# Optimization experiments

Hardware: AMD Instinct MI355X
Metric: run time of the kernel (lower is better)

## Reference

```python
import jax, jax.numpy as jnp
import numpy as np

NEG_SLOPE = 0.01  # torch LeakyReLU default

def setup_inputs() -> dict:
    key = jax.random.key(0)
    ks = jax.random.split(key, 16)
    B, T = 256, 168
    LAG, LAT, WS, H = 168, 128, 64, 1024
    def lin(kw, kb, out_f, in_f):
        bound = 1.0 / np.sqrt(in_f)
        W = jax.random.uniform(kw, (out_f, in_f), jnp.float32, -bound, bound)
        b = jax.random.uniform(kb, (out_f,), jnp.float32, -bound, bound)
        return W, b
    W1, b1 = lin(ks[0], ks[1], 64, LAG)
    W2, b2 = lin(ks[2], ks[3], LAT, 64)
    W3, b3 = lin(ks[4], ks[5], H, LAT)
    bound = 1.0 / np.sqrt(H)
    Wih = jax.random.uniform(ks[6], (3 * H, WS), jnp.float32, -bound, bound)
    Whh = jax.random.uniform(ks[7], (3 * H, H), jnp.float32, -bound, bound)
    bih = jax.random.uniform(ks[8], (3 * H,), jnp.float32, -bound, bound)
    bhh = jax.random.uniform(ks[9], (3 * H,), jnp.float32, -bound, bound)
    Wo, bo = lin(ks[10], ks[11], 1, H)
    lag = jax.random.normal(ks[12], (B, LAG), jnp.float32)
    curr = jax.random.normal(ks[13], (T, B, WS), jnp.float32)
    return dict(lag=lag, curr=curr, W1=W1, b1=b1, W2=W2, b2=b2, W3=W3, b3=b3,
                Wih=Wih, Whh=Whh, bih=bih, bhh=bhh, Wo=Wo, bo=bo)

def _leaky(x):
    return jnp.where(x >= 0, x, NEG_SLOPE * x)

def reference(lag, curr, W1, b1, W2, b2, W3, b3, Wih, Whh, bih, bhh, Wo, bo):
    # Encoder MLP: lag -> 64 -> latent -> hidden (leaky relu after first two)
    h = _leaky(lag @ W1.T + b1)
    h = _leaky(h @ W2.T + b2)
    h0 = h @ W3.T + b3  # [B, H]
    H = h0.shape[-1]

    def step(h_t, x_t):
        gi = x_t @ Wih.T + bih          # [B, 3H]
        gh = h_t @ Whh.T + bhh          # [B, 3H]
        ir, iz, inn = jnp.split(gi, 3, axis=-1)
        hr, hz, hn = jnp.split(gh, 3, axis=-1)
        r = jax.nn.sigmoid(ir + hr)
        z = jax.nn.sigmoid(iz + hz)
        n = jnp.tanh(inn + r * hn)
        h_new = (1.0 - z) * n + z * h_t
        return h_new, h_new

    _, hs = jax.lax.scan(step, h0, curr)          # hs: [T, B, H]
    preds = jnp.squeeze(hs @ Wo.T + bo, -1)       # [T, B]
    return preds.T                                 # [B, T]
```

## Files before the change

### kernel.cpp

```cpp
#include <hip/hip_runtime.h>
#include <hip/hip_bf16.h>
#include <cstdint>
#include <cstddef>

typedef _Float16 half8 __attribute__((ext_vector_type(8)));
typedef _Float16 half4 __attribute__((ext_vector_type(4)));
typedef float floatx4 __attribute__((ext_vector_type(4)));
typedef unsigned long long u64;

#define B_ 256
#define T_ 168
#define H_ 1024
#define WS_ 64
#define LAG_ 168
#define LAT_ 128

__device__ __forceinline__ float fast_sigmoid(float x) {
    return __builtin_amdgcn_rcpf(1.f + __expf(-x));
}
__device__ __forceinline__ float fast_tanh(float x) {
    return 1.f - 2.f * __builtin_amdgcn_rcpf(__expf(2.f * x) + 1.f);
}

__global__ void cvt_f32_f16_v4(const float4* __restrict__ src, half4* __restrict__ dst, int n4) {
    int i = blockIdx.x * blockDim.x + threadIdx.x;
    if (i < n4) {
        float4 v = src[i];
        half4 o;
        o[0] = (_Float16)v.x; o[1] = (_Float16)v.y;
        o[2] = (_Float16)v.z; o[3] = (_Float16)v.w;
        dst[i] = o;
    }
}

__global__ void enc12(const float* __restrict__ in, const float* __restrict__ W,
                      const float* __restrict__ bias, float* __restrict__ outb, int infeat) {
    int r = blockIdx.x, j = threadIdx.x;
    const float* row = in + (size_t)r * infeat;
    const float* w   = W  + (size_t)j * infeat;
    float s = bias[j];
    for (int k = 0; k < infeat; ++k) s += row[k] * w[k];
    outb[(size_t)r * blockDim.x + j] = (s >= 0.f) ? s : 0.01f * s;
}

__global__ void enc3(const float* __restrict__ h2, const float* __restrict__ W3,
                     const float* __restrict__ b3, float* __restrict__ hprev32,
                     _Float16* __restrict__ h0f16) {
    __shared__ float s[LAT_];
    int r = blockIdx.x;
    if (threadIdx.x < LAT_) s[threadIdx.x] = h2[(size_t)r * LAT_ + threadIdx.x];
    __syncthreads();
    for (int j = threadIdx.x; j < H_; j += 256) {
        const float* w = W3 + (size_t)j * LAT_;
        float acc = b3[j];
        #pragma unroll 8
        for (int k = 0; k < LAT_; ++k) acc += s[k] * w[k];
        hprev32[(size_t)r * H_ + j] = acc;
        h0f16[(size_t)r * H_ + j]   = (_Float16)acc;
    }
}

__global__ __launch_bounds__(256, 1) void gru_persistent(
    _Float16* __restrict__ hbuf,
    const float* __restrict__ hprev32, const _Float16* __restrict__ whh16,
    const _Float16* __restrict__ wih16, const _Float16* __restrict__ x16,
    const float* __restrict__ bih, const float* __restrict__ bhh,
    const float* __restrict__ Wo, float* __restrict__ partials,
    unsigned* __restrict__ bar)
{
    __shared__ __align__(16) _Float16 Ash[16 * 1032];
    __shared__ __align__(16) _Float16 Wsh[192 * 72];
    __shared__ __align__(16) _Float16 Hsh[4 * 256];

    const int tid  = threadIdx.x;
    const int w    = tid >> 6;
    const int lane = tid & 63;
    const int m16  = lane & 15;
    const int quad = lane >> 4;
    const int pi   = blockIdx.x & 15;
    const int qi   = blockIdx.x >> 4;
    const int pi16 = pi << 4;
    const int u    = (qi << 6) + (w << 4) + m16;

    for (int idx = tid; idx < 1536; idx += 256) {
        int rowl = idx >> 3, ch = idx & 7;
        int g = rowl >> 6, ru = rowl & 63;
        *(uint4*)(&Wsh[rowl * 72 + (ch << 3)]) =
            *(const uint4*)(wih16 + (size_t)(((g << 10) + (qi << 6) + ru) << 6) + (ch << 3));
    }

    half8 br[32], bz[32];
    {
        const _Float16* p0 = whh16 + ((size_t)u << 10) + (quad << 3);
        const _Float16* p1 = whh16 + ((size_t)(H_ + u) << 10) + (quad << 3);
        #pragma unroll
        for (int c = 0; c < 32; ++c) br[c] = *(const half8*)(p0 + (c << 5));
        #pragma unroll
        for (int c = 0; c < 32; ++c) bz[c] = *(const half8*)(p1 + (c << 5));
    }
    const _Float16* bnp = whh16 + ((size_t)(2 * H_ + u) << 10) + (quad << 3);

    const float b_r  = bih[u]          + bhh[u];
    const float b_z  = bih[H_ + u]     + bhh[H_ + u];
    const float b_in = bih[2 * H_ + u];
    const float b_hn = bhh[2 * H_ + u];
    const float wo_u = Wo[u];

    float hreg[4];
    #pragma unroll
    for (int i = 0; i < 4; ++i)
        hreg[i] = hprev32[((size_t)(pi16 + (quad << 2) + i) << 10) + u];

    __syncthreads();

    unsigned* flag_self       = bar + ((((pi << 4) | qi) << 2 | w) << 4);
    const unsigned* flag_peer = bar + ((((pi << 4) | (lane >> 2)) << 2 | (lane & 3)) << 4);
    const int srow = tid >> 4;
    const int sch  = tid & 15;
    const int prow = lane >> 2;
    const int pc4  = lane & 3;

    for (int t = 0; t < T_; ++t) {
        const _Float16* hsrc = hbuf + (size_t)(t & 3) * (B_ * H_);
        _Float16*       hdst = hbuf + (size_t)((t + 1) & 3) * (B_ * H_);

        half8 ax0 = *(const half8*)(x16 + (((size_t)t << 8) + pi16 + m16) * WS_ + (quad << 3));
        half8 ax1 = *(const half8*)(x16 + (((size_t)t << 8) + pi16 + m16) * WS_ + 32 + (quad << 3));
        half8 bnA[8], bnB[8];
        #pragma unroll
        for (int j = 0; j < 8; ++j) bnA[j] = *(const half8*)(bnp + (j << 5));

        const unsigned need = (unsigned)t;
        u64 rdy = 0;

        while ((rdy & 0xFFFFull) != 0xFFFFull) {
            unsigned f = __hip_atomic_load(flag_peer, __ATOMIC_RELAXED, __HIP_MEMORY_SCOPE_AGENT);
            rdy |= __ballot(f >= need);
            if ((rdy & 0xFFFFull) != 0xFFFFull) __builtin_amdgcn_s_sleep(1);
        }
        u64 va0, va1, va2, va3;
        {
            const _Float16* s = hsrc + ((size_t)(pi16 + srow) << 10) + (sch << 4);
            va0 = __hip_atomic_load((const u64*)(s + 0),  __ATOMIC_RELAXED, __HIP_MEMORY_SCOPE_AGENT);
            va1 = __hip_atomic_load((const u64*)(s + 4),  __ATOMIC_RELAXED, __HIP_MEMORY_SCOPE_AGENT);
            va2 = __hip_atomic_load((const u64*)(s + 8),  __ATOMIC_RELAXED, __HIP_MEMORY_SCOPE_AGENT);
            va3 = __hip_atomic_load((const u64*)(s + 12), __ATOMIC_RELAXED, __HIP_MEMORY_SCOPE_AGENT);
        }

        floatx4 acc_r  = {b_r,  b_r,  b_r,  b_r };
        floatx4 acc_z  = {b_z,  b_z,  b_z,  b_z };
        floatx4 acc_in = {b_in, b_in, b_in, b_in};
        floatx4 acc_hn = {b_hn, b_hn, b_hn, b_hn};

        {
            half8 p0 = *(const half8*)(&Wsh[((w << 4) + m16) * 72        + (quad << 3)]);
            half8 p1 = *(const half8*)(&Wsh[(64 + (w << 4) + m16) * 72   + (quad << 3)]);
            half8 p2 = *(const half8*)(&Wsh[(128 + (w << 4) + m16) * 72  + (quad << 3)]);
            acc_r  = __builtin_amdgcn_mfma_f32_16x16x32_f16(ax0, p0, acc_r,  0, 0, 0);
            acc_z  = __builtin_amdgcn_mfma_f32_16x16x32_f16(ax0, p1, acc_z,  0, 0, 0);
            acc_in = __builtin_amdgcn_mfma_f32_16x16x32_f16(ax0, p2, acc_in, 0, 0, 0);
            half8 q0 = *(const half8*)(&Wsh[((w << 4) + m16) * 72        + 32 + (quad << 3)]);
            half8 q1 = *(const half8*)(&Wsh[(64 + (w << 4) + m16) * 72   + 32 + (quad << 3)]);
            half8 q2 = *(const half8*)(&Wsh[(128 + (w << 4) + m16) * 72  + 32 + (quad << 3)]);
            acc_r  = __builtin_amdgcn_mfma_f32_16x16x32_f16(ax1, q0, acc_r,  0, 0, 0);
            acc_z  = __builtin_amdgcn_mfma_f32_16x16x32_f16(ax1, q1, acc_z,  0, 0, 0);
            acc_in = __builtin_amdgcn_mfma_f32_16x16x32_f16(ax1, q2, acc_in, 0, 0, 0);
        }

        #pragma unroll
        for (int g = 0; g < 4; ++g) {
            {
                _Float16* d = &Ash[srow * 1032 + (g << 8) + (sch << 4)];
                *(u64*)(d + 0)  = va0;
                *(u64*)(d + 4)  = va1;
                *(u64*)(d + 8)  = va2;
                *(u64*)(d + 12) = va3;
            }
            __syncthreads();
            if (g < 3) {
                const u64 mask = 0xFFFFull << ((g + 1) << 4);
                while ((rdy & mask) != mask) {
                    unsigned f = __hip_atomic_load(flag_peer, __ATOMIC_RELAXED, __HIP_MEMORY_SCOPE_AGENT);
                    rdy |= __ballot(f >= need);
                    if ((rdy & mask) != mask) __builtin_amdgcn_s_sleep(1);
                }
                const _Float16* s = hsrc + ((size_t)(pi16 + srow) << 10) + ((g + 1) << 8) + (sch << 4);
                va0 = __hip_atomic_load((const u64*)(s + 0),  __ATOMIC_RELAXED, __HIP_MEMORY_SCOPE_AGENT);
                va1 = __hip_atomic_load((const u64*)(s + 4),  __ATOMIC_RELAXED, __HIP_MEMORY_SCOPE_AGENT);
                va2 = __hip_atomic_load((const u64*)(s + 8),  __ATOMIC_RELAXED, __HIP_MEMORY_SCOPE_AGENT);
                va3 = __hip_atomic_load((const u64*)(s + 12), __ATOMIC_RELAXED, __HIP_MEMORY_SCOPE_AGENT);
                #pragma unroll
                for (int j = 0; j < 8; ++j)
                    bnB[j] = *(const half8*)(bnp + ((((g + 1) << 3) + j) << 5));
            }
            #pragma unroll
            for (int j = 0; j < 8; ++j) {
                const int c = (g << 3) + j;
                half8 a = *(const half8*)(&Ash[m16 * 1032 + (c << 5) + (quad << 3)]);
                acc_r  = __builtin_amdgcn_mfma_f32_16x16x32_f16(a, br[c], acc_r,  0, 0, 0);
                acc_z  = __builtin_amdgcn_mfma_f32_16x16x32_f16(a, bz[c], acc_z,  0, 0, 0);
                acc_hn = __builtin_amdgcn_mfma_f32_16x16x32_f16(a, bnA[j], acc_hn, 0, 0, 0);
            }
            if (g < 3) {
                #pragma unroll
                for (int j = 0; j < 8; ++j) bnA[j] = bnB[j];
            }
        }

        float pv[4];
        #pragma unroll
        for (int i = 0; i < 4; ++i) {
            float rg = fast_sigmoid(acc_r[i]);
            float zg = fast_sigmoid(acc_z[i]);
            float ng = fast_tanh(acc_in[i] + rg * acc_hn[i]);
            float hn2 = (1.f - zg) * ng + zg * hreg[i];
            hreg[i] = hn2;
            pv[i] = hn2 * wo_u;
            Hsh[(w << 8) + ((quad << 2) + i) * 16 + m16] = (_Float16)hn2;
        }
        __threadfence_block();
        {
            u64 hv = *(const u64*)(&Hsh[(w << 8) + prow * 16 + (pc4 << 2)]);
            __hip_atomic_store(
                (u64*)(hdst + ((size_t)(pi16 + prow) << 10) + (qi << 6) + (w << 4) + (pc4 << 2)),
                hv, __ATOMIC_RELAXED, __HIP_MEMORY_SCOPE_AGENT);
        }
        asm volatile("s_waitcnt vmcnt(0)" ::: "memory");
        if (lane == 0)
            __hip_atomic_store(flag_self, (unsigned)(t + 1),
                               __ATOMIC_RELAXED, __HIP_MEMORY_SCOPE_AGENT);
        #pragma unroll
        for (int m = 1; m < 16; m <<= 1) {
            #pragma unroll
            for (int i = 0; i < 4; ++i) pv[i] += __shfl_xor(pv[i], m);
        }
        if (m16 == 0) {
            #pragma unroll
            for (int i = 0; i < 4; ++i)
                partials[((size_t)t * B_ + pi16 + (quad << 2) + i) * 64 + (qi << 2) + w] = pv[i];
        }
    }
}

__global__ void out_reduce(const float* __restrict__ partials, const float* __restrict__ bo,
                           float* __restrict__ out) {
    int t = blockIdx.x, r = threadIdx.x;
    const float* p = partials + ((size_t)t * B_ + r) * 64;
    float s = 0.f;
    #pragma unroll
    for (int i = 0; i < 64; ++i) s += p[i];
    out[(size_t)r * T_ + t] = s + bo[0];
}

extern "C" void kernel_launch(void* const* d_in, const int* in_sizes, int n_in,
                              void* d_out, int out_size, void* d_ws, size_t ws_size,
                              hipStream_t stream) {
    const float* lag  = (const float*)d_in[0];
    const float* curr = (const float*)d_in[1];
    const float* W1   = (const float*)d_in[2];
    const float* b1   = (const float*)d_in[3];
    const float* W2   = (const float*)d_in[4];
    const float* b2   = (const float*)d_in[5];
    const float* W3   = (const float*)d_in[6];
    const float* b3   = (const float*)d_in[7];
    const float* Wih  = (const float*)d_in[8];
    const float* Whh  = (const float*)d_in[9];
    const float* bih  = (const float*)d_in[10];
    const float* bhh  = (const float*)d_in[11];
    const float* Wo   = (const float*)d_in[12];
    const float* bo   = (const float*)d_in[13];
    float* out = (float*)d_out;

    char* ws = (char*)d_ws;
    size_t off = 0;
    auto alloc = [&](size_t bytes) -> void* {
        void* p = ws + off;
        off += (bytes + 255) & ~(size_t)255;
        return p;
    };
    _Float16* whh16 = (_Float16*)alloc((size_t)3 * H_ * H_ * 2);
    _Float16* wih16 = (_Float16*)alloc((size_t)3 * H_ * WS_ * 2);
    _Float16* x16   = (_Float16*)alloc((size_t)T_ * B_ * WS_ * 2);
    _Float16* hbuf  = (_Float16*)alloc((size_t)4 * B_ * H_ * 2);
    float* hprev32  = (float*)alloc((size_t)B_ * H_ * 4);
    float* h1       = (float*)alloc((size_t)B_ * 64 * 4);
    float* h2       = (float*)alloc((size_t)B_ * LAT_ * 4);
    float* partials = (float*)alloc((size_t)T_ * B_ * 64 * 4);
    unsigned* bar   = (unsigned*)alloc(81920);

    hipMemsetAsync(bar, 0, 81920, stream);

    int n4;
    n4 = 3 * H_ * H_ / 4;
    cvt_f32_f16_v4<<<(n4 + 255) / 256, 256, 0, stream>>>((const float4*)Whh, (half4*)whh16, n4);
    n4 = 3 * H_ * WS_ / 4;
    cvt_f32_f16_v4<<<(n4 + 255) / 256, 256, 0, stream>>>((const float4*)Wih, (half4*)wih16, n4);
    n4 = T_ * B_ * WS_ / 4;
    cvt_f32_f16_v4<<<(n4 + 255) / 256, 256, 0, stream>>>((const float4*)curr, (half4*)x16, n4);

    enc12<<<B_, 64, 0, stream>>>(lag, W1, b1, h1, LAG_);
    enc12<<<B_, LAT_, 0, stream>>>(h1, W2, b2, h2, 64);
    enc3<<<B_, 256, 0, stream>>>(h2, W3, b3, hprev32, hbuf);

    gru_persistent<<<dim3(256), dim3(256), 0, stream>>>(
        hbuf, hprev32, whh16, wih16, x16, bih, bhh, Wo, partials, bar);

    out_reduce<<<T_, B_, 0, stream>>>(partials, bo, out);
}
```

Baseline: 812.3 us.

## Split GRU persistent kernel into 512 two-wave blocks covering 32 hidden units

The persistent GRU kernel now launches 512 blocks of 128 threads instead of 256 blocks of 256 threads. Each block owns 32 hidden units rather than 64, with smaller shared buffers for the input weights and staged outputs. The flag layout, the h-staging copy width and the mapping of blocks to batch tiles are reworked to match. The aim is smaller blocks, lighter __syncthreads, and possibly two blocks per CU. The cost is that every block still stages the full 16x1024 h tile, so global/L2 traffic for h roughly doubles. It also requires all 512 blocks to be co-resident for the spin barrier to make progress.

```diff
diff --git a/kernel.cpp b/kernel.cpp
--- a/kernel.cpp
+++ b/kernel.cpp
@@ -60,7 +60,7 @@
     }
 }
 
-__global__ __launch_bounds__(256, 1) void gru_persistent(
+__global__ __launch_bounds__(128, 1) void gru_persistent(
     _Float16* __restrict__ hbuf,
     const float* __restrict__ hprev32, const _Float16* __restrict__ whh16,
     const _Float16* __restrict__ wih16, const _Float16* __restrict__ x16,
@@ -69,24 +69,26 @@
     unsigned* __restrict__ bar)
 {
     __shared__ __align__(16) _Float16 Ash[16 * 1032];
-    __shared__ __align__(16) _Float16 Wsh[192 * 72];
-    __shared__ __align__(16) _Float16 Hsh[4 * 256];
+    __shared__ __align__(16) _Float16 Wsh[96 * 72];
+    __shared__ __align__(16) _Float16 Hsh[2 * 256];
 
     const int tid  = threadIdx.x;
     const int w    = tid >> 6;
     const int lane = tid & 63;
     const int m16  = lane & 15;
     const int quad = lane >> 4;
-    const int pi   = blockIdx.x & 15;
-    const int qi   = blockIdx.x >> 4;
+    const int blk  = blockIdx.x;
+    const int pi   = ((blk & 15) + (blk >> 8)) & 15;
+    const int qi   = (blk >> 4) & 31;
     const int pi16 = pi << 4;
-    const int u    = (qi << 6) + (w << 4) + m16;
-
-    for (int idx = tid; idx < 1536; idx += 256) {
+    const int u    = (qi << 5) + (w << 4) + m16;
+    const int slice_self = (qi << 1) | w;
+
+    for (int idx = tid; idx < 768; idx += 128) {
         int rowl = idx >> 3, ch = idx & 7;
-        int g = rowl >> 6, ru = rowl & 63;
+        int g = rowl >> 5, ru = rowl & 31;
         *(uint4*)(&Wsh[rowl * 72 + (ch << 3)]) =
-            *(const uint4*)(wih16 + (size_t)(((g << 10) + (qi << 6) + ru) << 6) + (ch << 3));
+            *(const uint4*)(wih16 + (size_t)(((g << 10) + (qi << 5) + ru) << 6) + (ch << 3));
     }
 
     half8 br[32], bz[32];
@@ -113,10 +115,10 @@
 
     __syncthreads();
 
-    unsigned* flag_self       = bar + ((((pi << 4) | qi) << 2 | w) << 4);
-    const unsigned* flag_peer = bar + ((((pi << 4) | (lane >> 2)) << 2 | (lane & 3)) << 4);
-    const int srow = tid >> 4;
-    const int sch  = tid & 15;
+    unsigned* flag_self       = bar + (((pi << 6) | slice_self) << 4);
+    const unsigned* flag_peer = bar + (((pi << 6) | lane) << 4);
+    const int srow = tid >> 3;
+    const int sch  = tid & 7;
     const int prow = lane >> 2;
     const int pc4  = lane & 3;
 
@@ -138,13 +140,12 @@
             rdy |= __ballot(f >= need);
             if ((rdy & 0xFFFFull) != 0xFFFFull) __builtin_amdgcn_s_sleep(1);
         }
-        u64 va0, va1, va2, va3;
+        u64 va[8];
         {
-            const _Float16* s = hsrc + ((size_t)(pi16 + srow) << 10) + (sch << 4);
-            va0 = __hip_atomic_load((const u64*)(s + 0),  __ATOMIC_RELAXED, __HIP_MEMORY_SCOPE_AGENT);
-            va1 = __hip_atomic_load((const u64*)(s + 4),  __ATOMIC_RELAXED, __HIP_MEMORY_SCOPE_AGENT);
-            va2 = __hip_atomic_load((const u64*)(s + 8),  __ATOMIC_RELAXED, __HIP_MEMORY_SCOPE_AGENT);
-            va3 = __hip_atomic_load((const u64*)(s + 12), __ATOMIC_RELAXED, __HIP_MEMORY_SCOPE_AGENT);
+            const _Float16* s = hsrc + ((size_t)(pi16 + srow) << 10) + (sch << 5);
+            #pragma unroll
+            for (int j = 0; j < 8; ++j)
+                va[j] = __hip_atomic_load((const u64*)(s + (j << 2)), __ATOMIC_RELAXED, __HIP_MEMORY_SCOPE_AGENT);
         }
 
         floatx4 acc_r  = {b_r,  b_r,  b_r,  b_r };
@@ -153,15 +154,15 @@
         floatx4 acc_hn = {b_hn, b_hn, b_hn, b_hn};
 
         {
-            half8 p0 = *(const half8*)(&Wsh[((w << 4) + m16) * 72        + (quad << 3)]);
-            half8 p1 = *(const half8*)(&Wsh[(64 + (w << 4) + m16) * 72   + (quad << 3)]);
-            half8 p2 = *(const half8*)(&Wsh[(128 + (w << 4) + m16) * 72  + (quad << 3)]);
+            half8 p0 = *(const half8*)(&Wsh[((w << 4) + m16) * 72       + (quad << 3)]);
+            half8 p1 = *(const half8*)(&Wsh[(32 + (w << 4) + m16) * 72  + (quad << 3)]);
+            half8 p2 = *(const half8*)(&Wsh[(64 + (w << 4) + m16) * 72  + (quad << 3)]);
             acc_r  = __builtin_amdgcn_mfma_f32_16x16x32_f16(ax0, p0, acc_r,  0, 0, 0);
             acc_z  = __builtin_amdgcn_mfma_f32_16x16x32_f16(ax0, p1, acc_z,  0, 0, 0);
             acc_in = __builtin_amdgcn_mfma_f32_16x16x32_f16(ax0, p2, acc_in, 0, 0, 0);
-            half8 q0 = *(const half8*)(&Wsh[((w << 4) + m16) * 72        + 32 + (quad << 3)]);
-            half8 q1 = *(const half8*)(&Wsh[(64 + (w << 4) + m16) * 72   + 32 + (quad << 3)]);
-            half8 q2 = *(const half8*)(&Wsh[(128 + (w << 4) + m16) * 72  + 32 + (quad << 3)]);
+            half8 q0 = *(const half8*)(&Wsh[((w << 4) + m16) * 72       + 32 + (quad << 3)]);
+            half8 q1 = *(const half8*)(&Wsh[(32 + (w << 4) + m16) * 72  + 32 + (quad << 3)]);
+            half8 q2 = *(const half8*)(&Wsh[(64 + (w << 4) + m16) * 72  + 32 + (quad << 3)]);
             acc_r  = __builtin_amdgcn_mfma_f32_16x16x32_f16(ax1, q0, acc_r,  0, 0, 0);
             acc_z  = __builtin_amdgcn_mfma_f32_16x16x32_f16(ax1, q1, acc_z,  0, 0, 0);
             acc_in = __builtin_amdgcn_mfma_f32_16x16x32_f16(ax1, q2, acc_in, 0, 0, 0);
@@ -170,11 +171,9 @@
         #pragma unroll
         for (int g = 0; g < 4; ++g) {
             {
-                _Float16* d = &Ash[srow * 1032 + (g << 8) + (sch << 4)];
-                *(u64*)(d + 0)  = va0;
-                *(u64*)(d + 4)  = va1;
-                *(u64*)(d + 8)  = va2;
-                *(u64*)(d + 12) = va3;
+                _Float16* d = &Ash[srow * 1032 + (g << 8) + (sch << 5)];
+                #pragma unroll
+                for (int j = 0; j < 8; ++j) *(u64*)(d + (j << 2)) = va[j];
             }
             __syncthreads();
             if (g < 3) {
@@ -184,11 +183,10 @@
                     rdy |= __ballot(f >= need);
                     if ((rdy & mask) != mask) __builtin_amdgcn_s_sleep(1);
                 }
-                const _Float16* s = hsrc + ((size_t)(pi16 + srow) << 10) + ((g + 1) << 8) + (sch << 4);
-                va0 = __hip_atomic_load((const u64*)(s + 0),  __ATOMIC_RELAXED, __HIP_MEMORY_SCOPE_AGENT);
-                va1 = __hip_atomic_load((const u64*)(s + 4),  __ATOMIC_RELAXED, __HIP_MEMORY_SCOPE_AGENT);
-                va2 = __hip_atomic_load((const u64*)(s + 8),  __ATOMIC_RELAXED, __HIP_MEMORY_SCOPE_AGENT);
-                va3 = __hip_atomic_load((const u64*)(s + 12), __ATOMIC_RELAXED, __HIP_MEMORY_SCOPE_AGENT);
+                const _Float16* s = hsrc + ((size_t)(pi16 + srow) << 10) + ((g + 1) << 8) + (sch << 5);
+                #pragma unroll
+                for (int j = 0; j < 8; ++j)
+                    va[j] = __hip_atomic_load((const u64*)(s + (j << 2)), __ATOMIC_RELAXED, __HIP_MEMORY_SCOPE_AGENT);
                 #pragma unroll
                 for (int j = 0; j < 8; ++j)
                     bnB[j] = *(const half8*)(bnp + ((((g + 1) << 3) + j) << 5));
@@ -222,7 +220,7 @@
         {
             u64 hv = *(const u64*)(&Hsh[(w << 8) + prow * 16 + (pc4 << 2)]);
             __hip_atomic_store(
-                (u64*)(hdst + ((size_t)(pi16 + prow) << 10) + (qi << 6) + (w << 4) + (pc4 << 2)),
+                (u64*)(hdst + ((size_t)(pi16 + prow) << 10) + (qi << 5) + (w << 4) + (pc4 << 2)),
                 hv, __ATOMIC_RELAXED, __HIP_MEMORY_SCOPE_AGENT);
         }
         asm volatile("s_waitcnt vmcnt(0)" ::: "memory");
@@ -237,7 +235,7 @@
         if (m16 == 0) {
             #pragma unroll
             for (int i = 0; i < 4; ++i)
-                partials[((size_t)t * B_ + pi16 + (quad << 2) + i) * 64 + (qi << 2) + w] = pv[i];
+                partials[((size_t)t * B_ + pi16 + (quad << 2) + i) * 64 + (qi << 1) + w] = pv[i];
         }
     }
 }
@@ -302,7 +300,7 @@
     enc12<<<B_, LAT_, 0, stream>>>(h1, W2, b2, h2, 64);
     enc3<<<B_, 256, 0, stream>>>(h2, W3, b3, hprev32, hbuf);
 
-    gru_persistent<<<dim3(256), dim3(256), 0, stream>>>(
+    gru_persistent<<<dim3(512), dim3(128), 0, stream>>>(
         hbuf, hprev32, whh16, wih16, x16, bih, bhh, Wo, partials, bar);
 
     out_reduce<<<T_, B_, 0, stream>>>(partials, bo, out);
```

Measured after the change: 1.390 ms. +71.1%, slower.

## Use per-slice flag waits and prefetch next-step readiness in GRU recurrence

Applied to the files above, without the earlier changes.

Replaces the wave-wide ballot spin on all 16 peer flags before each group with a per-thread check of only the flag guarding the hidden-state slice it loads. Hidden-state loads are issued speculatively and reissued only if that slice was not marked ready. Peer flags for the next timestep are polled right after this block publishes its own flag, overlapping that poll with the shuffle reduction. The aim is to cut time spent in the serialized cross-block barrier on the critical path. The cost is possible redundant reloads and more per-thread divergent spinning.

```diff
diff --git a/kernel.cpp b/kernel.cpp
--- a/kernel.cpp
+++ b/kernel.cpp
@@ -114,30 +114,19 @@
     __syncthreads();
 
     unsigned* flag_self       = bar + ((((pi << 4) | qi) << 2 | w) << 4);
-    const unsigned* flag_peer = bar + ((((pi << 4) | (lane >> 2)) << 2 | (lane & 3)) << 4);
+    const unsigned* flag_peer = bar + (((pi << 6) | lane) << 4);
     const int srow = tid >> 4;
     const int sch  = tid & 15;
     const int prow = lane >> 2;
     const int pc4  = lane & 3;
 
+    u64 rdy = 0;
+
     for (int t = 0; t < T_; ++t) {
         const _Float16* hsrc = hbuf + (size_t)(t & 3) * (B_ * H_);
         _Float16*       hdst = hbuf + (size_t)((t + 1) & 3) * (B_ * H_);
-
-        half8 ax0 = *(const half8*)(x16 + (((size_t)t << 8) + pi16 + m16) * WS_ + (quad << 3));
-        half8 ax1 = *(const half8*)(x16 + (((size_t)t << 8) + pi16 + m16) * WS_ + 32 + (quad << 3));
-        half8 bnA[8], bnB[8];
-        #pragma unroll
-        for (int j = 0; j < 8; ++j) bnA[j] = *(const half8*)(bnp + (j << 5));
-
         const unsigned need = (unsigned)t;
-        u64 rdy = 0;
-
-        while ((rdy & 0xFFFFull) != 0xFFFFull) {
-            unsigned f = __hip_atomic_load(flag_peer, __ATOMIC_RELAXED, __HIP_MEMORY_SCOPE_AGENT);
-            rdy |= __ballot(f >= need);
-            if ((rdy & 0xFFFFull) != 0xFFFFull) __builtin_amdgcn_s_sleep(1);
-        }
+
         u64 va0, va1, va2, va3;
         {
             const _Float16* s = hsrc + ((size_t)(pi16 + srow) << 10) + (sch << 4);
@@ -146,6 +135,11 @@
             va2 = __hip_atomic_load((const u64*)(s + 8),  __ATOMIC_RELAXED, __HIP_MEMORY_SCOPE_AGENT);
             va3 = __hip_atomic_load((const u64*)(s + 12), __ATOMIC_RELAXED, __HIP_MEMORY_SCOPE_AGENT);
         }
+        half8 ax0 = *(const half8*)(x16 + (((size_t)t << 8) + pi16 + m16) * WS_ + (quad << 3));
+        half8 ax1 = *(const half8*)(x16 + (((size_t)t << 8) + pi16 + m16) * WS_ + 32 + (quad << 3));
+        half8 bnA[8], bnB[8];
+        #pragma unroll
+        for (int j = 0; j < 8; ++j) bnA[j] = *(const half8*)(bnp + (j << 5));
 
         floatx4 acc_r  = {b_r,  b_r,  b_r,  b_r };
         floatx4 acc_z  = {b_z,  b_z,  b_z,  b_z };
@@ -170,6 +164,22 @@
         #pragma unroll
         for (int g = 0; g < 4; ++g) {
             {
+                const int myslice = (g << 4) + sch;
+                if (!((rdy >> myslice) & 1)) {
+                    const unsigned* fp = bar + (((pi << 6) | myslice) << 4);
+                    unsigned f = __hip_atomic_load(fp, __ATOMIC_RELAXED, __HIP_MEMORY_SCOPE_AGENT);
+                    while (f < need) {
+                        __builtin_amdgcn_s_sleep(1);
+                        f = __hip_atomic_load(fp, __ATOMIC_RELAXED, __HIP_MEMORY_SCOPE_AGENT);
+                    }
+                    const _Float16* s = hsrc + ((size_t)(pi16 + srow) << 10) + (g << 8) + (sch << 4);
+                    va0 = __hip_atomic_load((const u64*)(s + 0),  __ATOMIC_RELAXED, __HIP_MEMORY_SCOPE_AGENT);
+                    va1 = __hip_atomic_load((const u64*)(s + 4),  __ATOMIC_RELAXED, __HIP_MEMORY_SCOPE_AGENT);
+                    va2 = __hip_atomic_load((const u64*)(s + 8),  __ATOMIC_RELAXED, __HIP_MEMORY_SCOPE_AGENT);
+                    va3 = __hip_atomic_load((const u64*)(s + 12), __ATOMIC_RELAXED, __HIP_MEMORY_SCOPE_AGENT);
+                }
+            }
+            {
                 _Float16* d = &Ash[srow * 1032 + (g << 8) + (sch << 4)];
                 *(u64*)(d + 0)  = va0;
                 *(u64*)(d + 4)  = va1;
@@ -178,12 +188,6 @@
             }
             __syncthreads();
             if (g < 3) {
-                const u64 mask = 0xFFFFull << ((g + 1) << 4);
-                while ((rdy & mask) != mask) {
-                    unsigned f = __hip_atomic_load(flag_peer, __ATOMIC_RELAXED, __HIP_MEMORY_SCOPE_AGENT);
-                    rdy |= __ballot(f >= need);
-                    if ((rdy & mask) != mask) __builtin_amdgcn_s_sleep(1);
-                }
                 const _Float16* s = hsrc + ((size_t)(pi16 + srow) << 10) + ((g + 1) << 8) + (sch << 4);
                 va0 = __hip_atomic_load((const u64*)(s + 0),  __ATOMIC_RELAXED, __HIP_MEMORY_SCOPE_AGENT);
                 va1 = __hip_atomic_load((const u64*)(s + 4),  __ATOMIC_RELAXED, __HIP_MEMORY_SCOPE_AGENT);
@@ -229,16 +233,28 @@
         if (lane == 0)
             __hip_atomic_store(flag_self, (unsigned)(t + 1),
                                __ATOMIC_RELAXED, __HIP_MEMORY_SCOPE_AGENT);
+
+        u64 rdy_next = 0;
+        unsigned f1 = 0;
+        if (t < T_ - 1)
+            f1 = __hip_atomic_load(flag_peer, __ATOMIC_RELAXED, __HIP_MEMORY_SCOPE_AGENT);
         #pragma unroll
         for (int m = 1; m < 16; m <<= 1) {
             #pragma unroll
             for (int i = 0; i < 4; ++i) pv[i] += __shfl_xor(pv[i], m);
         }
+        if (t < T_ - 1)
+            rdy_next = __ballot(f1 >= (unsigned)(t + 1));
         if (m16 == 0) {
             #pragma unroll
             for (int i = 0; i < 4; ++i)
                 partials[((size_t)t * B_ + pi16 + (quad << 2) + i) * 64 + (qi << 2) + w] = pv[i];
         }
+        if (t < T_ - 1 && rdy_next != ~0ull) {
+            unsigned f2 = __hip_atomic_load(flag_peer, __ATOMIC_RELAXED, __HIP_MEMORY_SCOPE_AGENT);
+            rdy_next |= __ballot(f2 >= (unsigned)(t + 1));
+        }
+        rdy = rdy_next;
     }
 }
 
```

After: 1.034 ms. 27.2% more time.
